# Optimization experiments

Hardware: AMD Instinct MI355X
Metric: run time of the kernel (lower is better)

The kernel has to match this reference:

```python
import jax, jax.numpy as jnp
import numpy as np

DROPOUT_P = 0.5
NUM_NODES = 50000


def _gcn_layer(x, W, b, src, dst, ew, num_nodes):
    # support = x @ W ; out = A_hat @ support + b, with A_hat given as edge list
    h = x @ W                               # [N, out_dim]
    msg = h[src] * ew[:, None]              # [E, out_dim]
    agg = jax.ops.segment_sum(msg, dst, num_segments=num_nodes)  # [N, out_dim]
    return agg + b


def setup_inputs() -> dict:
    key = jax.random.key(0)
    ks = jax.random.split(key, 8)
    N, E, F_in, H, C = NUM_NODES, 800000, 512, 128, 64
    x = jax.random.normal(ks[0], (N, F_in), dtype=jnp.float32)
    edge_weight = jax.random.uniform(ks[1], (E,), dtype=jnp.float32)
    W1 = jax.random.normal(ks[2], (F_in, H), dtype=jnp.float32) * (1.0 / np.sqrt(F_in))
    b1 = jax.random.normal(ks[3], (H,), dtype=jnp.float32) * 0.01
    W2 = jax.random.normal(ks[4], (H, C), dtype=jnp.float32) * (1.0 / np.sqrt(H))
    b2 = jax.random.normal(ks[5], (C,), dtype=jnp.float32) * 0.01
    drop_mask = jax.random.uniform(ks[6], (N, H), dtype=jnp.float32)
    edge_index = jax.random.randint(ks[7], (2, E), 0, N, dtype=jnp.int32)
    return {"x": x, "edge_weight": edge_weight, "W1": W1, "b1": b1,
            "W2": W2, "b2": b2, "drop_mask": drop_mask, "edge_index": edge_index}


def reference(x, edge_weight, W1, b1, W2, b2, drop_mask, edge_index):
    src, dst = edge_index[0], edge_index[1]
    h = _gcn_layer(x, W1, b1, src, dst, edge_weight, NUM_NODES)
    h = jax.nn.relu(h)
    # deterministic inverted dropout using precomputed uniform mask
    keep = (drop_mask >= DROPOUT_P).astype(h.dtype)
    h = h * keep / (1.0 - DROPOUT_P)
    h = _gcn_layer(h, W2, b2, src, dst, edge_weight, NUM_NODES)
    return jax.nn.log_softmax(h, axis=1)
```

## Files before the change

kernel.cpp:

```cpp
#include <hip/hip_runtime.h>
#include <cstdint>
#include <cstddef>

constexpr int FIN = 512;
constexpr int HD  = 128;
constexpr int CD  = 64;

typedef __attribute__((ext_vector_type(8))) short short8;
typedef __attribute__((ext_vector_type(4))) float f32x4;

__device__ inline unsigned short f2bf(float f) {
  unsigned int u = __float_as_uint(f);
  u += 0x7fffu + ((u >> 16) & 1u);
  return (unsigned short)(u >> 16);
}
__device__ inline float bf_lo(unsigned int v) { return __uint_as_float(v << 16); }
__device__ inline float bf_hi(unsigned int v) { return __uint_as_float(v & 0xffff0000u); }
__device__ inline float bf1(unsigned short v) { return __uint_as_float((unsigned int)v << 16); }


__global__ __launch_bounds__(256) void prep(const float* __restrict__ W1,
                                            const float* __restrict__ W2,
                                            unsigned short* __restrict__ w1t,
                                            unsigned short* __restrict__ w2t,
                                            int* __restrict__ cnt, int n) {
  int idx = blockIdx.x * 256 + threadIdx.x;
  if (idx < FIN * HD) {
    int k = idx >> 7, c = idx & 127;
    w1t[(size_t)c * FIN + k] = f2bf(W1[idx]);
  } else if (idx < FIN * HD + HD * CD) {
    int j = idx - FIN * HD;
    int k = j >> 6, c = j & 63;
    w2t[(size_t)c * HD + k] = f2bf(W2[j]);
  }
  if (idx < n) cnt[idx] = 0;
}


__global__ __launch_bounds__(256) void hist_kernel(const int* __restrict__ dst, int E,
                                                   int* __restrict__ cnt) {
  int i = blockIdx.x * 256 + threadIdx.x;
  if (i < E) atomicAdd(&cnt[dst[i]], 1);
}


__global__ __launch_bounds__(256) void scan_a(const int* __restrict__ cnt,
                                              int* __restrict__ bs, int n) {
  __shared__ int sh[256];
  int t = threadIdx.x;
  int base = blockIdx.x * 2048;
  int s = 0;
#pragma unroll
  for (int j = 0; j < 8; ++j) {
    int idx = base + j * 256 + t;
    if (idx < n) s += cnt[idx];
  }
  sh[t] = s;
  __syncthreads();
  for (int o = 128; o > 0; o >>= 1) {
    if (t < o) sh[t] += sh[t + o];
    __syncthreads();
  }
  if (t == 0) bs[blockIdx.x] = sh[0];
}

__global__ __launch_bounds__(256) void scan_c(const int* __restrict__ cnt,
                                              const int* __restrict__ bs,
                                              int* __restrict__ off,
                                              int* __restrict__ cur, int n) {
  __shared__ int sh[256];
  __shared__ int sbase;
  const int t   = threadIdx.x;
  const int bid = blockIdx.x;
  if (t < 64) {
    int v = (t < bid) ? bs[t] : 0;
#pragma unroll
    for (int o = 32; o > 0; o >>= 1) v += __shfl_xor(v, o, 64);
    if (t == 0) sbase = v;
  }
  const int base = bid * 2048 + t * 8;
  int v[8];
  int local = 0;
#pragma unroll
  for (int j = 0; j < 8; ++j) {
    v[j] = (base + j < n) ? cnt[base + j] : 0;
    local += v[j];
  }
  sh[t] = local;
  __syncthreads();
  for (int o = 1; o < 256; o <<= 1) {
    int u = (t >= o) ? sh[t - o] : 0;
    __syncthreads();
    sh[t] += u;
    __syncthreads();
  }
  int run = sbase + sh[t] - local;
#pragma unroll
  for (int j = 0; j < 8; ++j) {
    if (base + j < n) { off[base + j] = run; cur[base + j] = run; }
    run += v[j];
  }
}


__global__ __launch_bounds__(256) void scatter_kernel(const int* __restrict__ src,
                                                      const int* __restrict__ dst,
                                                      const float* __restrict__ ew, int E,
                                                      int* __restrict__ cur,
                                                      int2* __restrict__ sew) {
  int i = blockIdx.x * 256 + threadIdx.x;
  if (i < E) {
    int d = dst[i];
    int p = atomicAdd(&cur[d], 1);
    sew[p] = make_int2(src[i], __float_as_int(ew[i]));
  }
}


__global__ __launch_bounds__(256) void gemm1_mfma(const float* __restrict__ x,
                                                  const unsigned short* __restrict__ w1t,
                                                  unsigned short* __restrict__ h1b, int M) {
  __shared__ unsigned short As[128][40];
  __shared__ unsigned short Bs[128][40];
  const int t    = threadIdx.x;
  const int wave = t >> 6;
  const int lane = t & 63;
  const int l15  = lane & 15;
  const int quad = lane >> 4;
  const int m0   = blockIdx.x * 128;

  const int sr = t >> 1;
  const int sk = (t & 1) * 16;

  const bool aok = (m0 + sr) < M;
  const float* xrow = x + (size_t)(m0 + sr) * FIN + sk;
  const unsigned short* brow = w1t + (size_t)sr * FIN + sk;

  f32x4 acc[2][8];
#pragma unroll
  for (int i = 0; i < 2; ++i)
#pragma unroll
    for (int j = 0; j < 8; ++j) acc[i][j] = (f32x4)0.f;

  for (int k0 = 0; k0 < FIN; k0 += 32) {
    float4 a0 = make_float4(0.f, 0.f, 0.f, 0.f), a1 = a0, a2 = a0, a3 = a0;
    if (aok) {
      a0 = *(const float4*)(xrow + k0);
      a1 = *(const float4*)(xrow + k0 + 4);
      a2 = *(const float4*)(xrow + k0 + 8);
      a3 = *(const float4*)(xrow + k0 + 12);
    }
    uint4 b0 = *(const uint4*)(brow + k0);
    uint4 b1 = *(const uint4*)(brow + k0 + 8);
    __syncthreads();
    unsigned short tmp[16];
    tmp[0]  = f2bf(a0.x); tmp[1]  = f2bf(a0.y); tmp[2]  = f2bf(a0.z); tmp[3]  = f2bf(a0.w);
    tmp[4]  = f2bf(a1.x); tmp[5]  = f2bf(a1.y); tmp[6]  = f2bf(a1.z); tmp[7]  = f2bf(a1.w);
    tmp[8]  = f2bf(a2.x); tmp[9]  = f2bf(a2.y); tmp[10] = f2bf(a2.z); tmp[11] = f2bf(a2.w);
    tmp[12] = f2bf(a3.x); tmp[13] = f2bf(a3.y); tmp[14] = f2bf(a3.z); tmp[15] = f2bf(a3.w);
    *(uint4*)&As[sr][sk]     = ((const uint4*)tmp)[0];
    *(uint4*)&As[sr][sk + 8] = ((const uint4*)tmp)[1];
    *(uint4*)&Bs[sr][sk]     = b0;
    *(uint4*)&Bs[sr][sk + 8] = b1;
    __syncthreads();
    short8 af0 = *(const short8*)&As[wave * 32 + l15][quad * 8];
    short8 af1 = *(const short8*)&As[wave * 32 + 16 + l15][quad * 8];
#pragma unroll
    for (int nt = 0; nt < 8; ++nt) {
      short8 bf = *(const short8*)&Bs[nt * 16 + l15][quad * 8];
      acc[0][nt] = __builtin_amdgcn_mfma_f32_16x16x32_bf16(af0, bf, acc[0][nt], 0, 0, 0);
      acc[1][nt] = __builtin_amdgcn_mfma_f32_16x16x32_bf16(af1, bf, acc[1][nt], 0, 0, 0);
    }
  }
#pragma unroll
  for (int mt = 0; mt < 2; ++mt) {
    const int row0 = m0 + wave * 32 + mt * 16 + quad * 4;
#pragma unroll
    for (int r = 0; r < 4; ++r) {
      int row = row0 + r;
      if (row < M) {
        unsigned short* orow = h1b + (size_t)row * HD + l15;
#pragma unroll
        for (int nt = 0; nt < 8; ++nt) orow[nt * 16] = f2bf(acc[mt][nt][r]);
      }
    }
  }
}


__global__ __launch_bounds__(256) void agg1_kernel(const unsigned int* __restrict__ h1b,
                                                   const float* __restrict__ b1,
                                                   const float* __restrict__ dm,
                                                   const int* __restrict__ off,
                                                   const int* __restrict__ cnt,
                                                   const int2* __restrict__ sew,
                                                   unsigned int* __restrict__ hbf, int N) {
  const int wave = threadIdx.x >> 6;
  const int lane = threadIdx.x & 63;
  const int node = blockIdx.x * 4 + wave;
  if (node >= N) return;
  const int start = off[node];
  const int deg   = cnt[node];
  const int2* ep  = sew + start;

  float a0 = 0.f, a1 = 0.f, c0 = 0.f, c1 = 0.f;
  float e0 = 0.f, e1 = 0.f, g0 = 0.f, g1 = 0.f;
  int e = 0;
  for (; e + 8 <= deg; e += 8) {
    int2 p0 = ep[e + 0], p1 = ep[e + 1], p2 = ep[e + 2], p3 = ep[e + 3];
    int2 p4 = ep[e + 4], p5 = ep[e + 5], p6 = ep[e + 6], p7 = ep[e + 7];
    unsigned int v0 = h1b[(size_t)p0.x * 64 + lane];
    unsigned int v1 = h1b[(size_t)p1.x * 64 + lane];
    unsigned int v2 = h1b[(size_t)p2.x * 64 + lane];
    unsigned int v3 = h1b[(size_t)p3.x * 64 + lane];
    unsigned int v4 = h1b[(size_t)p4.x * 64 + lane];
    unsigned int v5 = h1b[(size_t)p5.x * 64 + lane];
    unsigned int v6 = h1b[(size_t)p6.x * 64 + lane];
    unsigned int v7 = h1b[(size_t)p7.x * 64 + lane];
    float w0 = __int_as_float(p0.y), w1 = __int_as_float(p1.y);
    float w2 = __int_as_float(p2.y), w3 = __int_as_float(p3.y);
    float w4 = __int_as_float(p4.y), w5 = __int_as_float(p5.y);
    float w6 = __int_as_float(p6.y), w7 = __int_as_float(p7.y);
    a0 = fmaf(bf_lo(v0), w0, a0); a1 = fmaf(bf_hi(v0), w0, a1);
    c0 = fmaf(bf_lo(v1), w1, c0); c1 = fmaf(bf_hi(v1), w1, c1);
    e0 = fmaf(bf_lo(v2), w2, e0); e1 = fmaf(bf_hi(v2), w2, e1);
    g0 = fmaf(bf_lo(v3), w3, g0); g1 = fmaf(bf_hi(v3), w3, g1);
    a0 = fmaf(bf_lo(v4), w4, a0); a1 = fmaf(bf_hi(v4), w4, a1);
    c0 = fmaf(bf_lo(v5), w5, c0); c1 = fmaf(bf_hi(v5), w5, c1);
    e0 = fmaf(bf_lo(v6), w6, e0); e1 = fmaf(bf_hi(v6), w6, e1);
    g0 = fmaf(bf_lo(v7), w7, g0); g1 = fmaf(bf_hi(v7), w7, g1);
  }
  for (; e + 4 <= deg; e += 4) {
    int2 p0 = ep[e + 0], p1 = ep[e + 1], p2 = ep[e + 2], p3 = ep[e + 3];
    unsigned int v0 = h1b[(size_t)p0.x * 64 + lane];
    unsigned int v1 = h1b[(size_t)p1.x * 64 + lane];
    unsigned int v2 = h1b[(size_t)p2.x * 64 + lane];
    unsigned int v3 = h1b[(size_t)p3.x * 64 + lane];
    float w0 = __int_as_float(p0.y), w1 = __int_as_float(p1.y);
    float w2 = __int_as_float(p2.y), w3 = __int_as_float(p3.y);
    a0 = fmaf(bf_lo(v0), w0, a0); a1 = fmaf(bf_hi(v0), w0, a1);
    c0 = fmaf(bf_lo(v1), w1, c0); c1 = fmaf(bf_hi(v1), w1, c1);
    e0 = fmaf(bf_lo(v2), w2, e0); e1 = fmaf(bf_hi(v2), w2, e1);
    g0 = fmaf(bf_lo(v3), w3, g0); g1 = fmaf(bf_hi(v3), w3, g1);
  }
  for (; e < deg; ++e) {
    int2 p = ep[e];
    unsigned int v = h1b[(size_t)p.x * 64 + lane];
    float w = __int_as_float(p.y);
    a0 = fmaf(bf_lo(v), w, a0); a1 = fmaf(bf_hi(v), w, a1);
  }
  a0 += c0 + e0 + g0; a1 += c1 + e1 + g1;

  const int f0 = lane * 2;
  float2 bb = *(const float2*)(b1 + f0);
  float2 dd = *(const float2*)(dm + (size_t)node * HD + f0);
  float r0 = fmaxf(a0 + bb.x, 0.f) * ((dd.x >= 0.5f) ? 2.0f : 0.0f);
  float r1 = fmaxf(a1 + bb.y, 0.f) * ((dd.y >= 0.5f) ? 2.0f : 0.0f);
  hbf[(size_t)node * 64 + lane] = (unsigned int)f2bf(r0) | ((unsigned int)f2bf(r1) << 16);
}


__global__ __launch_bounds__(256) void gemm2_mfma(const unsigned short* __restrict__ hbf,
                                                  const unsigned short* __restrict__ w2t,
                                                  unsigned short* __restrict__ h2b, int M) {
  __shared__ unsigned short As[128][40];
  __shared__ unsigned short Bs[64][40];
  const int t    = threadIdx.x;
  const int wave = t >> 6;
  const int lane = t & 63;
  const int l15  = lane & 15;
  const int quad = lane >> 4;
  const int m0   = blockIdx.x * 128;

  const int sr = t >> 1;
  const int sk = (t & 1) * 16;
  const int rb = t >> 2;
  const int kb = (t & 3) * 8;

  const bool aok = (m0 + sr) < M;
  const unsigned short* arow = hbf + (size_t)(m0 + sr) * HD + sk;
  const unsigned short* brow = w2t + (size_t)rb * HD + kb;

  f32x4 acc[2][4];
#pragma unroll
  for (int i = 0; i < 2; ++i)
#pragma unroll
    for (int j = 0; j < 4; ++j) acc[i][j] = (f32x4)0.f;

  for (int k0 = 0; k0 < HD; k0 += 32) {
    uint4 av0 = make_uint4(0, 0, 0, 0), av1 = av0;
    if (aok) {
      av0 = *(const uint4*)(arow + k0);
      av1 = *(const uint4*)(arow + k0 + 8);
    }
    uint4 bv = *(const uint4*)(brow + k0);
    __syncthreads();
    *(uint4*)&As[sr][sk]     = av0;
    *(uint4*)&As[sr][sk + 8] = av1;
    *(uint4*)&Bs[rb][kb]     = bv;
    __syncthreads();
    short8 af0 = *(const short8*)&As[wave * 32 + l15][quad * 8];
    short8 af1 = *(const short8*)&As[wave * 32 + 16 + l15][quad * 8];
#pragma unroll
    for (int nt = 0; nt < 4; ++nt) {
      short8 bf = *(const short8*)&Bs[nt * 16 + l15][quad * 8];
      acc[0][nt] = __builtin_amdgcn_mfma_f32_16x16x32_bf16(af0, bf, acc[0][nt], 0, 0, 0);
      acc[1][nt] = __builtin_amdgcn_mfma_f32_16x16x32_bf16(af1, bf, acc[1][nt], 0, 0, 0);
    }
  }
#pragma unroll
  for (int mt = 0; mt < 2; ++mt) {
    const int row0 = m0 + wave * 32 + mt * 16 + quad * 4;
#pragma unroll
    for (int r = 0; r < 4; ++r) {
      int row = row0 + r;
      if (row < M) {
        unsigned short* orow = h2b + (size_t)row * CD + l15;
#pragma unroll
        for (int nt = 0; nt < 4; ++nt) orow[nt * 16] = f2bf(acc[mt][nt][r]);
      }
    }
  }
}


__global__ __launch_bounds__(256) void agg2_kernel(const unsigned short* __restrict__ h2b,
                                                   const float* __restrict__ b2,
                                                   const int* __restrict__ off,
                                                   const int* __restrict__ cnt,
                                                   const int2* __restrict__ sew,
                                                   float* __restrict__ out, int N) {
  const int wave = threadIdx.x >> 6;
  const int c    = threadIdx.x & 63;
  const int node = blockIdx.x * 4 + wave;
  if (node >= N) return;
  const int start = off[node];
  const int deg   = cnt[node];
  const int2* ep  = sew + start;

  float acc = b2[c], a1 = 0.f, a2 = 0.f, a3 = 0.f;
  int e = 0;
  for (; e + 8 <= deg; e += 8) {
    int2 p0 = ep[e + 0], p1 = ep[e + 1], p2 = ep[e + 2], p3 = ep[e + 3];
    int2 p4 = ep[e + 4], p5 = ep[e + 5], p6 = ep[e + 6], p7 = ep[e + 7];
    float v0 = bf1(h2b[(size_t)p0.x * CD + c]);
    float v1 = bf1(h2b[(size_t)p1.x * CD + c]);
    float v2 = bf1(h2b[(size_t)p2.x * CD + c]);
    float v3 = bf1(h2b[(size_t)p3.x * CD + c]);
    float v4 = bf1(h2b[(size_t)p4.x * CD + c]);
    float v5 = bf1(h2b[(size_t)p5.x * CD + c]);
    float v6 = bf1(h2b[(size_t)p6.x * CD + c]);
    float v7 = bf1(h2b[(size_t)p7.x * CD + c]);
    acc = fmaf(v0, __int_as_float(p0.y), acc);
    a1  = fmaf(v1, __int_as_float(p1.y), a1);
    a2  = fmaf(v2, __int_as_float(p2.y), a2);
    a3  = fmaf(v3, __int_as_float(p3.y), a3);
    acc = fmaf(v4, __int_as_float(p4.y), acc);
    a1  = fmaf(v5, __int_as_float(p5.y), a1);
    a2  = fmaf(v6, __int_as_float(p6.y), a2);
    a3  = fmaf(v7, __int_as_float(p7.y), a3);
  }
  for (; e + 4 <= deg; e += 4) {
    int2 p0 = ep[e + 0], p1 = ep[e + 1], p2 = ep[e + 2], p3 = ep[e + 3];
    float v0 = bf1(h2b[(size_t)p0.x * CD + c]);
    float v1 = bf1(h2b[(size_t)p1.x * CD + c]);
    float v2 = bf1(h2b[(size_t)p2.x * CD + c]);
    float v3 = bf1(h2b[(size_t)p3.x * CD + c]);
    acc = fmaf(v0, __int_as_float(p0.y), acc);
    a1  = fmaf(v1, __int_as_float(p1.y), a1);
    a2  = fmaf(v2, __int_as_float(p2.y), a2);
    a3  = fmaf(v3, __int_as_float(p3.y), a3);
  }
  for (; e < deg; ++e) {
    int2 p = ep[e];
    acc = fmaf(bf1(h2b[(size_t)p.x * CD + c]), __int_as_float(p.y), acc);
  }
  acc += a1 + a2 + a3;

  float m = acc;
#pragma unroll
  for (int o = 32; o > 0; o >>= 1) m = fmaxf(m, __shfl_xor(m, o, 64));
  float ex = __expf(acc - m);
  float ssum = ex;
#pragma unroll
  for (int o = 32; o > 0; o >>= 1) ssum += __shfl_xor(ssum, o, 64);
  out[(size_t)node * CD + c] = (acc - m) - __logf(ssum);
}


extern "C" void kernel_launch(void* const* d_in, const int* in_sizes, int n_in,
                              void* d_out, int out_size, void* d_ws, size_t ws_size,
                              hipStream_t stream) {
  const float* x  = (const float*)d_in[0];
  const float* ew = (const float*)d_in[1];
  const float* W1 = (const float*)d_in[2];
  const float* b1 = (const float*)d_in[3];
  const float* W2 = (const float*)d_in[4];
  const float* b2 = (const float*)d_in[5];
  const float* dm = (const float*)d_in[6];
  const int*   ei = (const int*)d_in[7];
  float* out = (float*)d_out;

  const int E = in_sizes[1];
  const int N = in_sizes[6] / HD;
  const int* srcp = ei;
  const int* dstp = ei + E;
  const int nb = (N + 2047) / 2048;

  uint8_t* w = (uint8_t*)d_ws;
  size_t o = 0;
  auto alloc = [&](size_t bytes) -> void* {
    void* p = w + o;
    o = (o + bytes + 255) & ~(size_t)255;
    return p;
  };
  int*   off    = (int*)alloc((size_t)N * 4);
  int*   cnt    = (int*)alloc((size_t)N * 4);
  int*   cur    = (int*)alloc((size_t)N * 4);
  int2*  sew    = (int2*)alloc((size_t)E * 8);
  unsigned short* h1b = (unsigned short*)alloc((size_t)N * HD * 2);
  unsigned int*   hbf = (unsigned int*)alloc((size_t)N * HD * 2);
  unsigned short* h2b = (unsigned short*)alloc((size_t)N * CD * 2);
  unsigned short* w1t = (unsigned short*)alloc((size_t)FIN * HD * 2);
  unsigned short* w2t = (unsigned short*)alloc((size_t)HD * CD * 2);
  int*   bsum   = (int*)alloc((size_t)nb * 4);

  const int prep_threads = FIN * HD + HD * CD;
  prep<<<(prep_threads + 255) / 256, 256, 0, stream>>>(W1, W2, w1t, w2t, cnt, N);
  hist_kernel<<<(E + 255) / 256, 256, 0, stream>>>(dstp, E, cnt);
  scan_a<<<nb, 256, 0, stream>>>(cnt, bsum, N);
  scan_c<<<nb, 256, 0, stream>>>(cnt, bsum, off, cur, N);
  scatter_kernel<<<(E + 255) / 256, 256, 0, stream>>>(srcp, dstp, ew, E, cur, sew);
  gemm1_mfma<<<(N + 127) / 128, 256, 0, stream>>>(x, w1t, h1b, N);
  agg1_kernel<<<(N + 3) / 4, 256, 0, stream>>>((const unsigned int*)h1b, b1, dm, off, cnt, sew, hbf, N);
  gemm2_mfma<<<(N + 127) / 128, 256, 0, stream>>>((const unsigned short*)hbf, w2t, h2b, N);
  agg2_kernel<<<(N + 3) / 4, 256, 0, stream>>>(h2b, b2, off, cnt, sew, out, N);
}
```

Before: 358.1 us.

## Fuse degree histogram into gemm1 and retile gemm1 to 64-row, K=64 tiles

Removes the standalone histogram kernel and folds its atomic degree counting into the start of gemm1, which now launches before the scan/scatter CSR build. gemm1 is retiled from 128-row blocks with K-step 32 to 64-row blocks with K-step 64, giving each wave one 16-row strip and twice as many blocks. This cuts one launch and lets the atomic traffic overlap with the GEMM. In exchange, each wave runs fewer MFMAs per B-fragment load, so B-operand reuse drops and W1 traffic rises.

```diff
diff --git a/kernel.cpp b/kernel.cpp
--- a/kernel.cpp
+++ b/kernel.cpp
@@ -37,13 +37,6 @@
 }
 
 
-__global__ __launch_bounds__(256) void hist_kernel(const int* __restrict__ dst, int E,
-                                                   int* __restrict__ cnt) {
-  int i = blockIdx.x * 256 + threadIdx.x;
-  if (i < E) atomicAdd(&cnt[dst[i]], 1);
-}
-
-
 __global__ __launch_bounds__(256) void scan_a(const int* __restrict__ cnt,
                                               int* __restrict__ bs, int n) {
   __shared__ int sh[256];
@@ -119,30 +112,38 @@
 
 __global__ __launch_bounds__(256) void gemm1_mfma(const float* __restrict__ x,
                                                   const unsigned short* __restrict__ w1t,
-                                                  unsigned short* __restrict__ h1b, int M) {
-  __shared__ unsigned short As[128][40];
-  __shared__ unsigned short Bs[128][40];
+                                                  unsigned short* __restrict__ h1b, int M,
+                                                  const int* __restrict__ dst, int E,
+                                                  int* __restrict__ cnt) {
+  {
+    const int stride = gridDim.x * 256;
+    for (int i = blockIdx.x * 256 + threadIdx.x; i < E; i += stride)
+      atomicAdd(&cnt[dst[i]], 1);
+  }
+
+  __shared__ unsigned short As[64][72];
+  __shared__ unsigned short Bs[128][72];
   const int t    = threadIdx.x;
   const int wave = t >> 6;
   const int lane = t & 63;
   const int l15  = lane & 15;
   const int quad = lane >> 4;
-  const int m0   = blockIdx.x * 128;
-
-  const int sr = t >> 1;
-  const int sk = (t & 1) * 16;
-
-  const bool aok = (m0 + sr) < M;
-  const float* xrow = x + (size_t)(m0 + sr) * FIN + sk;
-  const unsigned short* brow = w1t + (size_t)sr * FIN + sk;
-
-  f32x4 acc[2][8];
-#pragma unroll
-  for (int i = 0; i < 2; ++i)
-#pragma unroll
-    for (int j = 0; j < 8; ++j) acc[i][j] = (f32x4)0.f;
-
-  for (int k0 = 0; k0 < FIN; k0 += 32) {
+  const int m0   = blockIdx.x * 64;
+
+  const int ar = t >> 2;
+  const int ak = (t & 3) * 16;
+  const int br = t >> 1;
+  const int bk = (t & 1) * 32;
+
+  const bool aok = (m0 + ar) < M;
+  const float* xrow = x + (size_t)(m0 + ar) * FIN + ak;
+  const unsigned short* brow = w1t + (size_t)br * FIN + bk;
+
+  f32x4 acc[8];
+#pragma unroll
+  for (int j = 0; j < 8; ++j) acc[j] = (f32x4)0.f;
+
+  for (int k0 = 0; k0 < FIN; k0 += 64) {
     float4 a0 = make_float4(0.f, 0.f, 0.f, 0.f), a1 = a0, a2 = a0, a3 = a0;
     if (aok) {
       a0 = *(const float4*)(xrow + k0);
@@ -152,37 +153,39 @@
     }
     uint4 b0 = *(const uint4*)(brow + k0);
     uint4 b1 = *(const uint4*)(brow + k0 + 8);
+    uint4 b2 = *(const uint4*)(brow + k0 + 16);
+    uint4 b3 = *(const uint4*)(brow + k0 + 24);
     __syncthreads();
     unsigned short tmp[16];
     tmp[0]  = f2bf(a0.x); tmp[1]  = f2bf(a0.y); tmp[2]  = f2bf(a0.z); tmp[3]  = f2bf(a0.w);
     tmp[4]  = f2bf(a1.x); tmp[5]  = f2bf(a1.y); tmp[6]  = f2bf(a1.z); tmp[7]  = f2bf(a1.w);
     tmp[8]  = f2bf(a2.x); tmp[9]  = f2bf(a2.y); tmp[10] = f2bf(a2.z); tmp[11] = f2bf(a2.w);
     tmp[12] = f2bf(a3.x); tmp[13] = f2bf(a3.y); tmp[14] = f2bf(a3.z); tmp[15] = f2bf(a3.w);
-    *(uint4*)&As[sr][sk]     = ((const uint4*)tmp)[0];
-    *(uint4*)&As[sr][sk + 8] = ((const uint4*)tmp)[1];
-    *(uint4*)&Bs[sr][sk]     = b0;
-    *(uint4*)&Bs[sr][sk + 8] = b1;
-    __syncthreads();
-    short8 af0 = *(const short8*)&As[wave * 32 + l15][quad * 8];
-    short8 af1 = *(const short8*)&As[wave * 32 + 16 + l15][quad * 8];
-#pragma unroll
-    for (int nt = 0; nt < 8; ++nt) {
-      short8 bf = *(const short8*)&Bs[nt * 16 + l15][quad * 8];
-      acc[0][nt] = __builtin_amdgcn_mfma_f32_16x16x32_bf16(af0, bf, acc[0][nt], 0, 0, 0);
-      acc[1][nt] = __builtin_amdgcn_mfma_f32_16x16x32_bf16(af1, bf, acc[1][nt], 0, 0, 0);
-    }
-  }
-#pragma unroll
-  for (int mt = 0; mt < 2; ++mt) {
-    const int row0 = m0 + wave * 32 + mt * 16 + quad * 4;
-#pragma unroll
-    for (int r = 0; r < 4; ++r) {
-      int row = row0 + r;
-      if (row < M) {
-        unsigned short* orow = h1b + (size_t)row * HD + l15;
-#pragma unroll
-        for (int nt = 0; nt < 8; ++nt) orow[nt * 16] = f2bf(acc[mt][nt][r]);
+    *(uint4*)&As[ar][ak]     = ((const uint4*)tmp)[0];
+    *(uint4*)&As[ar][ak + 8] = ((const uint4*)tmp)[1];
+    *(uint4*)&Bs[br][bk]      = b0;
+    *(uint4*)&Bs[br][bk + 8]  = b1;
+    *(uint4*)&Bs[br][bk + 16] = b2;
+    *(uint4*)&Bs[br][bk + 24] = b3;
+    __syncthreads();
+#pragma unroll
+    for (int ks = 0; ks < 64; ks += 32) {
+      short8 af = *(const short8*)&As[wave * 16 + l15][ks + quad * 8];
+#pragma unroll
+      for (int nt = 0; nt < 8; ++nt) {
+        short8 bf = *(const short8*)&Bs[nt * 16 + l15][ks + quad * 8];
+        acc[nt] = __builtin_amdgcn_mfma_f32_16x16x32_bf16(af, bf, acc[nt], 0, 0, 0);
       }
+    }
+  }
+  const int row0 = m0 + wave * 16 + quad * 4;
+#pragma unroll
+  for (int r = 0; r < 4; ++r) {
+    int row = row0 + r;
+    if (row < M) {
+      unsigned short* orow = h1b + (size_t)row * HD + l15;
+#pragma unroll
+      for (int nt = 0; nt < 8; ++nt) orow[nt * 16] = f2bf(acc[nt][r]);
     }
   }
 }
@@ -427,11 +430,10 @@
 
   const int prep_threads = FIN * HD + HD * CD;
   prep<<<(prep_threads + 255) / 256, 256, 0, stream>>>(W1, W2, w1t, w2t, cnt, N);
-  hist_kernel<<<(E + 255) / 256, 256, 0, stream>>>(dstp, E, cnt);
+  gemm1_mfma<<<(N + 63) / 64, 256, 0, stream>>>(x, w1t, h1b, N, dstp, E, cnt);
   scan_a<<<nb, 256, 0, stream>>>(cnt, bsum, N);
   scan_c<<<nb, 256, 0, stream>>>(cnt, bsum, off, cur, N);
   scatter_kernel<<<(E + 255) / 256, 256, 0, stream>>>(srcp, dstp, ew, E, cur, sew);
-  gemm1_mfma<<<(N + 127) / 128, 256, 0, stream>>>(x, w1t, h1b, N);
   agg1_kernel<<<(N + 3) / 4, 256, 0, stream>>>((const unsigned int*)h1b, b1, dm, off, cnt, sew, hbf, N);
   gemm2_mfma<<<(N + 127) / 128, 256, 0, stream>>>((const unsigned short*)hbf, w2t, h2b, N);
   agg2_kernel<<<(N + 3) / 4, 256, 0, stream>>>(h2b, b2, off, cnt, sew, out, N);
```

Result: no change. 361.2 us (+0.9%).

## Replicate histogram and cursor counters to spread atomic contention across copies

Applied to the files above, without the earlier changes.

The degree histogram and the CSR scatter cursors are split into 8 per-block-group replicas, so atomics on the same destination node are spread across separate addresses. The scans sum the replicas and give each replica its own base offset, and a separate degree array now replaces cnt in the aggregation kernels. The bf16 packing in gemm1 now builds uint32 pairs directly instead of going through a short array, and gemm1 is launched earlier in the stream. The cost is 8x the counter memory and more reads in the scan kernels, plus a larger zeroing launch in prep.

```diff
diff --git a/kernel.cpp b/kernel.cpp
--- a/kernel.cpp
+++ b/kernel.cpp
@@ -5,6 +5,7 @@
 constexpr int FIN = 512;
 constexpr int HD  = 128;
 constexpr int CD  = 64;
+constexpr int NREP = 8;
 
 typedef __attribute__((ext_vector_type(8))) short short8;
 typedef __attribute__((ext_vector_type(4))) float f32x4;
@@ -14,6 +15,9 @@
   u += 0x7fffu + ((u >> 16) & 1u);
   return (unsigned short)(u >> 16);
 }
+__device__ inline unsigned int pk2(float lo, float hi) {
+  return (unsigned int)f2bf(lo) | ((unsigned int)f2bf(hi) << 16);
+}
 __device__ inline float bf_lo(unsigned int v) { return __uint_as_float(v << 16); }
 __device__ inline float bf_hi(unsigned int v) { return __uint_as_float(v & 0xffff0000u); }
 __device__ inline float bf1(unsigned short v) { return __uint_as_float((unsigned int)v << 16); }
@@ -23,7 +27,7 @@
                                             const float* __restrict__ W2,
                                             unsigned short* __restrict__ w1t,
                                             unsigned short* __restrict__ w2t,
-                                            int* __restrict__ cnt, int n) {
+                                            int* __restrict__ cnt, int n8) {
   int idx = blockIdx.x * 256 + threadIdx.x;
   if (idx < FIN * HD) {
     int k = idx >> 7, c = idx & 127;
@@ -33,14 +37,15 @@
     int k = j >> 6, c = j & 63;
     w2t[(size_t)c * HD + k] = f2bf(W2[j]);
   }
-  if (idx < n) cnt[idx] = 0;
+  if (idx < n8) cnt[idx] = 0;
 }
 
 
 __global__ __launch_bounds__(256) void hist_kernel(const int* __restrict__ dst, int E,
-                                                   int* __restrict__ cnt) {
+                                                   int* __restrict__ cnt, int Nn) {
+  int* rep = cnt + (size_t)(blockIdx.x & (NREP - 1)) * Nn;
   int i = blockIdx.x * 256 + threadIdx.x;
-  if (i < E) atomicAdd(&cnt[dst[i]], 1);
+  if (i < E) atomicAdd(&rep[dst[i]], 1);
 }
 
 
@@ -53,7 +58,10 @@
 #pragma unroll
   for (int j = 0; j < 8; ++j) {
     int idx = base + j * 256 + t;
-    if (idx < n) s += cnt[idx];
+    if (idx < n) {
+#pragma unroll
+      for (int r = 0; r < NREP; ++r) s += cnt[(size_t)r * n + idx];
+    }
   }
   sh[t] = s;
   __syncthreads();
@@ -67,7 +75,8 @@
 __global__ __launch_bounds__(256) void scan_c(const int* __restrict__ cnt,
                                               const int* __restrict__ bs,
                                               int* __restrict__ off,
-                                              int* __restrict__ cur, int n) {
+                                              int* __restrict__ cur8,
+                                              int* __restrict__ deg, int n) {
   __shared__ int sh[256];
   __shared__ int sbase;
   const int t   = threadIdx.x;
@@ -83,8 +92,13 @@
   int local = 0;
 #pragma unroll
   for (int j = 0; j < 8; ++j) {
-    v[j] = (base + j < n) ? cnt[base + j] : 0;
-    local += v[j];
+    int s = 0;
+    if (base + j < n) {
+#pragma unroll
+      for (int r = 0; r < NREP; ++r) s += cnt[(size_t)r * n + base + j];
+    }
+    v[j] = s;
+    local += s;
   }
   sh[t] = local;
   __syncthreads();
@@ -97,7 +111,17 @@
   int run = sbase + sh[t] - local;
 #pragma unroll
   for (int j = 0; j < 8; ++j) {
-    if (base + j < n) { off[base + j] = run; cur[base + j] = run; }
+    int idx = base + j;
+    if (idx < n) {
+      off[idx] = run;
+      deg[idx] = v[j];
+      int b = run;
+#pragma unroll
+      for (int r = 0; r < NREP; ++r) {
+        cur8[(size_t)r * n + idx] = b;
+        b += cnt[(size_t)r * n + idx];
+      }
+    }
     run += v[j];
   }
 }
@@ -106,12 +130,13 @@
 __global__ __launch_bounds__(256) void scatter_kernel(const int* __restrict__ src,
                                                       const int* __restrict__ dst,
                                                       const float* __restrict__ ew, int E,
-                                                      int* __restrict__ cur,
+                                                      int* __restrict__ cur8, int Nn,
                                                       int2* __restrict__ sew) {
+  int* rep = cur8 + (size_t)(blockIdx.x & (NREP - 1)) * Nn;
   int i = blockIdx.x * 256 + threadIdx.x;
   if (i < E) {
     int d = dst[i];
-    int p = atomicAdd(&cur[d], 1);
+    int p = atomicAdd(&rep[d], 1);
     sew[p] = make_int2(src[i], __float_as_int(ew[i]));
   }
 }
@@ -153,13 +178,13 @@
     uint4 b0 = *(const uint4*)(brow + k0);
     uint4 b1 = *(const uint4*)(brow + k0 + 8);
     __syncthreads();
-    unsigned short tmp[16];
-    tmp[0]  = f2bf(a0.x); tmp[1]  = f2bf(a0.y); tmp[2]  = f2bf(a0.z); tmp[3]  = f2bf(a0.w);
-    tmp[4]  = f2bf(a1.x); tmp[5]  = f2bf(a1.y); tmp[6]  = f2bf(a1.z); tmp[7]  = f2bf(a1.w);
-    tmp[8]  = f2bf(a2.x); tmp[9]  = f2bf(a2.y); tmp[10] = f2bf(a2.z); tmp[11] = f2bf(a2.w);
-    tmp[12] = f2bf(a3.x); tmp[13] = f2bf(a3.y); tmp[14] = f2bf(a3.z); tmp[15] = f2bf(a3.w);
-    *(uint4*)&As[sr][sk]     = ((const uint4*)tmp)[0];
-    *(uint4*)&As[sr][sk + 8] = ((const uint4*)tmp)[1];
+    uint4 av0, av1;
+    av0.x = pk2(a0.x, a0.y); av0.y = pk2(a0.z, a0.w);
+    av0.z = pk2(a1.x, a1.y); av0.w = pk2(a1.z, a1.w);
+    av1.x = pk2(a2.x, a2.y); av1.y = pk2(a2.z, a2.w);
+    av1.z = pk2(a3.x, a3.y); av1.w = pk2(a3.z, a3.w);
+    *(uint4*)&As[sr][sk]     = av0;
+    *(uint4*)&As[sr][sk + 8] = av1;
     *(uint4*)&Bs[sr][sk]     = b0;
     *(uint4*)&Bs[sr][sk + 8] = b1;
     __syncthreads();
@@ -415,8 +440,9 @@
     return p;
   };
   int*   off    = (int*)alloc((size_t)N * 4);
-  int*   cnt    = (int*)alloc((size_t)N * 4);
-  int*   cur    = (int*)alloc((size_t)N * 4);
+  int*   cnt    = (int*)alloc((size_t)NREP * N * 4);
+  int*   cur8   = (int*)alloc((size_t)NREP * N * 4);
+  int*   deg    = (int*)alloc((size_t)N * 4);
   int2*  sew    = (int2*)alloc((size_t)E * 8);
   unsigned short* h1b = (unsigned short*)alloc((size_t)N * HD * 2);
   unsigned int*   hbf = (unsigned int*)alloc((size_t)N * HD * 2);
@@ -425,14 +451,15 @@
   unsigned short* w2t = (unsigned short*)alloc((size_t)HD * CD * 2);
   int*   bsum   = (int*)alloc((size_t)nb * 4);
 
-  const int prep_threads = FIN * HD + HD * CD;
-  prep<<<(prep_threads + 255) / 256, 256, 0, stream>>>(W1, W2, w1t, w2t, cnt, N);
-  hist_kernel<<<(E + 255) / 256, 256, 0, stream>>>(dstp, E, cnt);
+  const int wcvt = FIN * HD + HD * CD;
+  const int prep_threads = (wcvt > NREP * N) ? wcvt : NREP * N;
+  prep<<<(prep_threads + 255) / 256, 256, 0, stream>>>(W1, W2, w1t, w2t, cnt, NREP * N);
+  hist_kernel<<<(E + 255) / 256, 256, 0, stream>>>(dstp, E, cnt, N);
+  gemm1_mfma<<<(N + 127) / 128, 256, 0, stream>>>(x, w1t, h1b, N);
   scan_a<<<nb, 256, 0, stream>>>(cnt, bsum, N);
-  scan_c<<<nb, 256, 0, stream>>>(cnt, bsum, off, cur, N);
-  scatter_kernel<<<(E + 255) / 256, 256, 0, stream>>>(srcp, dstp, ew, E, cur, sew);
-  gemm1_mfma<<<(N + 127) / 128, 256, 0, stream>>>(x, w1t, h1b, N);
-  agg1_kernel<<<(N + 3) / 4, 256, 0, stream>>>((const unsigned int*)h1b, b1, dm, off, cnt, sew, hbf, N);
+  scan_c<<<nb, 256, 0, stream>>>(cnt, bsum, off, cur8, deg, N);
+  scatter_kernel<<<(E + 255) / 256, 256, 0, stream>>>(srcp, dstp, ew, E, cur8, N, sew);
+  agg1_kernel<<<(N + 3) / 4, 256, 0, stream>>>((const unsigned int*)h1b, b1, dm, off, deg, sew, hbf, N);
   gemm2_mfma<<<(N + 127) / 128, 256, 0, stream>>>((const unsigned short*)hbf, w2t, h2b, N);
-  agg2_kernel<<<(N + 3) / 4, 256, 0, stream>>>(h2b, b2, off, cnt, sew, out, N);
-}
+  agg2_kernel<<<(N + 3) / 4, 256, 0, stream>>>(h2b, b2, off, deg, sew, out, N);
+}
```

Result: slower. 374.4 us (+4.5%).
